# Performance work log

Hardware: AMD Instinct MI355X
Metric: run time of the kernel (lower is better)

The kernel has to match this reference:

```python
import jax, jax.numpy as jnp
import numpy as np

NUM_GROUPS = 32
EPS = 1e-6


def group_norm(x, gamma, beta):
    # x: [B, C, H, W]
    B, C, H, W = x.shape
    xg = x.reshape(B, NUM_GROUPS, C // NUM_GROUPS, H, W)
    mean = jnp.mean(xg, axis=(2, 3, 4), keepdims=True)
    var = jnp.var(xg, axis=(2, 3, 4), keepdims=True)
    xn = ((xg - mean) * jax.lax.rsqrt(var + EPS)).reshape(B, C, H, W)
    return xn * gamma[None, :, None, None] + beta[None, :, None, None]


def conv1x1(x, w, b):
    # x: [B, C, H, W], w: [O, C], b: [O]  (1x1 conv == channel matmul)
    return jnp.einsum('oc,bchw->bohw', w, x) + b[None, :, None, None]


def setup_inputs() -> dict:
    key = jax.random.key(0)
    ks = jax.random.split(key, 10)
    B, C, H, W = 16, 512, 32, 32
    s = 1.0 / np.sqrt(C)
    inp = {
        'hidden_states': jax.random.normal(ks[0], (B, C, H, W), dtype=jnp.float32),
        'norm_gamma': jnp.ones((C,), dtype=jnp.float32),
        'norm_beta': jnp.zeros((C,), dtype=jnp.float32),
        'wq': jax.random.normal(ks[1], (C, C), dtype=jnp.float32) * s,
        'bq': jnp.zeros((C,), dtype=jnp.float32),
        'wk': jax.random.normal(ks[2], (C, C), dtype=jnp.float32) * s,
        'bk': jnp.zeros((C,), dtype=jnp.float32),
        'wv': jax.random.normal(ks[3], (C, C), dtype=jnp.float32) * s,
        'bv': jnp.zeros((C,), dtype=jnp.float32),
        'wo': jax.random.normal(ks[4], (C, C), dtype=jnp.float32) * s,
        'bo': jnp.zeros((C,), dtype=jnp.float32),
    }
    return inp


def reference(hidden_states, norm_gamma, norm_beta, wq, bq, wk, bk, wv, bv, wo, bo):
    residual = hidden_states
    h = group_norm(hidden_states, norm_gamma, norm_beta)
    q = conv1x1(h, wq, bq)  # [B, C, H, W]
    k = conv1x1(h, wk, bk)
    v = conv1x1(h, wv, bv)
    B, C, H, W = q.shape
    N = H * W
    qf = q.reshape(B, C, N)  # [B, C, N]
    kf = k.reshape(B, C, N)
    vf = v.reshape(B, C, N)
    scale = float(C) ** (-0.5)
    # attn_weights[b, i, j] = sum_c q[b,c,i] * k[b,c,j]
    attn = jnp.einsum('bci,bcj->bij', qf, kf) * scale
    attn = jax.nn.softmax(attn, axis=2)
    # out[b, c, i] = sum_j v[b,c,j] * attn[b,i,j]
    out = jnp.einsum('bcj,bij->bci', vf, attn).reshape(B, C, H, W)
    out = conv1x1(out, wo, bo)
    return residual + out
```

## Files before the change

### kernel.cpp

```cpp
#include <hip/hip_runtime.h>

typedef __attribute__((ext_vector_type(4))) float f32x4;
typedef __attribute__((ext_vector_type(8))) __bf16 bf16x8;
typedef __attribute__((ext_vector_type(4))) unsigned short us4;
typedef __attribute__((ext_vector_type(8))) unsigned short us8;

#define B_  16
#define C_  512
#define N_  1024
#define G_  32
#define GS  16

__device__ inline unsigned short f2bf(float f) {
  unsigned u = __builtin_bit_cast(unsigned, f);
  u += 0x7fffu + ((u >> 16) & 1u);
  return (unsigned short)(u >> 16);
}

#define GLOAD_LDS16(gp, lp) __builtin_amdgcn_global_load_lds( \
    (const __attribute__((address_space(1))) unsigned int*)(gp), \
    (__attribute__((address_space(3))) unsigned int*)(lp), 16, 0, 0)

__global__ __launch_bounds__(256) void gn_stats(const float* __restrict__ x,
                                                float* __restrict__ stats) {
  int bg = blockIdx.x;
  const float* xp = x + (long)bg * (GS * N_);
  int tid = threadIdx.x;
  float s = 0.f, ss = 0.f;
  for (int i = tid * 4; i < GS * N_; i += 1024) {
    f32x4 v = *(const f32x4*)&xp[i];
    s += v.x + v.y + v.z + v.w;
    ss += v.x * v.x + v.y * v.y + v.z * v.z + v.w * v.w;
  }
  __shared__ float r1[256], r2[256];
  r1[tid] = s; r2[tid] = ss; __syncthreads();
  for (int off = 128; off > 0; off >>= 1) {
    if (tid < off) { r1[tid] += r1[tid + off]; r2[tid] += r2[tid + off]; }
    __syncthreads();
  }
  if (tid == 0) {
    float mean = r1[0] * (1.f / (GS * N_));
    float var  = r2[0] * (1.f / (GS * N_)) - mean * mean;
    stats[bg * 2]     = mean;
    stats[bg * 2 + 1] = rsqrtf(var + 1e-6f);
  }
}

__global__ __launch_bounds__(256) void gn_apply(const float* __restrict__ x,
                                                const float* __restrict__ stats,
                                                const float* __restrict__ gamma,
                                                const float* __restrict__ beta,
                                                unsigned short* __restrict__ ht) {
  int b = blockIdx.z, ct = blockIdx.y, nt = blockIdx.x;
  int c0 = ct * 64, n0 = nt * 64;
  int tid = threadIdx.x;
  __shared__ unsigned short L[64 * 68];
  const float* xp = x + ((long)b * C_ + c0) * N_ + n0;
#pragma unroll
  for (int i = 0; i < 4; ++i) {
    int li = tid + i * 256;
    int row = li >> 4;
    int col4 = (li & 15) * 4;
    f32x4 v = *(const f32x4*)&xp[(long)row * N_ + col4];
    int c = c0 + row;
    float mean = stats[(b * G_ + (c >> 4)) * 2];
    float rstd = stats[(b * G_ + (c >> 4)) * 2 + 1];
    float gm = gamma[c] * rstd;
    float bt = beta[c] - mean * gm;
    us4 o;
    o.x = f2bf(v.x * gm + bt); o.y = f2bf(v.y * gm + bt);
    o.z = f2bf(v.z * gm + bt); o.w = f2bf(v.w * gm + bt);
    *(us4*)&L[row * 68 + col4] = o;
  }
  __syncthreads();
#pragma unroll
  for (int i = 0; i < 2; ++i) {
    int s = tid + i * 256;
    int n = s >> 3;
    int cs = (s & 7) * 8;
    us8 o;
#pragma unroll
    for (int j = 0; j < 8; ++j) o[j] = L[(cs + j) * 68 + n];
    *(us8*)&ht[((long)b * N_ + n0 + n) * C_ + c0 + cs] = o;
  }
}

__global__ __launch_bounds__(256) void convert_w(const float* __restrict__ wq, const float* __restrict__ wk,
                                                 const float* __restrict__ wo,
                                                 const float* __restrict__ bq, const float* __restrict__ bk,
                                                 const float* __restrict__ bv,
                                                 unsigned short* __restrict__ wqk,
                                                 unsigned short* __restrict__ wob, float* __restrict__ bqk,
                                                 float* __restrict__ bvo) {
  long bid = blockIdx.x;
  int tid = threadIdx.x;
  long i = bid * 256 + tid;
  if (i < C_ * C_) {
    wqk[i]           = f2bf(wq[i]);
    wqk[C_ * C_ + i] = f2bf(wk[i]);
    wob[i]           = f2bf(wo[i]);
  }
  if (i < C_) { bqk[i] = bq[i]; bqk[C_ + i] = bk[i]; }
  if (bid >= 1024) {
    int o = (int)(bid - 1024) * 256 + tid;
    const float* wr = wo + (long)o * 512;
    float acc = 0.f;
    for (int c = 0; c < 512; c += 4) {
      f32x4 w4 = *(const f32x4*)&wr[c];
      f32x4 b4 = *(const f32x4*)&bv[c];
      acc += w4.x * b4.x + w4.y * b4.y + w4.z * b4.z + w4.w * b4.w;
    }
    bvo[o] = acc;
  }
}

__global__ __launch_bounds__(256) void transpose_wv(const float* __restrict__ wv,
                                                    unsigned short* __restrict__ wvT) {
  int c0 = blockIdx.x * 64, k0 = blockIdx.y * 64;
  int tid = threadIdx.x;
  __shared__ float Lt[64][65];
#pragma unroll
  for (int i = 0; i < 4; ++i) {
    int lin = tid + i * 256;
    int rr = lin >> 4;
    int q4 = (lin & 15) * 4;
    f32x4 v = *(const f32x4*)&wv[(long)(c0 + rr) * 512 + k0 + q4];
    Lt[q4 + 0][rr] = v.x; Lt[q4 + 1][rr] = v.y;
    Lt[q4 + 2][rr] = v.z; Lt[q4 + 3][rr] = v.w;
  }
  __syncthreads();
#pragma unroll
  for (int i = 0; i < 2; ++i) {
    int lin = tid + i * 256;
    int kk = lin >> 3;
    int cc = (lin & 7) * 8;
    us8 o;
#pragma unroll
    for (int j = 0; j < 8; ++j) o[j] = f2bf(Lt[kk][cc + j]);
    *(us8*)&wvT[(long)(k0 + kk) * 512 + c0 + cc] = o;
  }
}

__device__ inline f32x4 mfma16(bf16x8 a, bf16x8 b, f32x4 c) {
  return __builtin_amdgcn_mfma_f32_16x16x32_bf16(a, b, c, 0, 0, 0);
}

__global__ __launch_bounds__(256) void wprod(const unsigned short* __restrict__ wob,
                                             const unsigned short* __restrict__ wvT,
                                             unsigned short* __restrict__ WVO) {
  int row0 = blockIdx.x * 64, col0 = blockIdx.y * 64;
  int tid = threadIdx.x, lane = tid & 63, w = tid >> 6;
  int lr = lane & 15, kh = (lane >> 4) * 8;
  f32x4 acc4[4];
#pragma unroll
  for (int n = 0; n < 4; ++n) acc4[n] = f32x4{0.f, 0.f, 0.f, 0.f};
  for (int k0 = 0; k0 < 512; k0 += 32) {
    bf16x8 af = *(const bf16x8*)&wob[(long)(row0 + w * 16 + lr) * 512 + k0 + kh];
#pragma unroll
    for (int n = 0; n < 4; ++n) {
      bf16x8 bf8 = *(const bf16x8*)&wvT[(long)(col0 + n * 16 + lr) * 512 + k0 + kh];
      acc4[n] = mfma16(af, bf8, acc4[n]);
    }
  }
  int rb = (lane >> 4) * 4;
#pragma unroll
  for (int n = 0; n < 4; ++n)
#pragma unroll
    for (int r = 0; r < 4; ++r)
      WVO[(long)(row0 + w * 16 + rb + r) * 512 + col0 + n * 16 + lr] = f2bf(acc4[n][r]);
}

__device__ inline int swz(int b) { return b ^ (((b >> 9) & 1) << 5); }

template<int NREP, int EPI, int XSWZ>
__global__ __launch_bounds__(512, 2) void gemm256(
    const unsigned short* __restrict__ A, long lda, long Az,
    const unsigned short* __restrict__ Bm, long ldb, long Bz,
    void* __restrict__ Dp, long ldd, long Dz,
    const float* __restrict__ bias, float scale, int K,
    const float* __restrict__ residual, float* __restrict__ rs) {
  constexpr int BN = NREP * 64;
  int bx = blockIdx.x, by = blockIdx.y, bz = blockIdx.z;
  if constexpr (XSWZ) {
    int lin = bx + 4 * (by + 4 * bz);
    int l2  = (lin & 7) * 32 + (lin >> 3);
    bx = l2 & 3; by = (l2 >> 2) & 3; bz = l2 >> 4;
  }
  const int z = bz;
  const long row0 = (long)bx * 256;
  const long col0 = (long)by * BN;
  const int tid  = threadIdx.x;
  const int lane = tid & 63;
  const int wave = tid >> 6;
  const int wm = wave >> 2;
  const int wn = wave & 3;
  const int lr = lane & 15;
  const int khb = (lane >> 4) * 16;

  __shared__ unsigned short Abuf[2][16384];
  __shared__ unsigned short Bbuf[2][NREP * 4096];
  __shared__ float sred[256];

  const unsigned short* Ab = A  + (long)z * Az;
  const unsigned short* Bb = Bm + (long)z * Bz;

  if constexpr (EPI == 7) {
    if (tid < 256) {
      const float* rp = rs + ((long)z * 1024 + row0 + tid) * 16;
      float s = 0.f;
#pragma unroll
      for (int i = 0; i < 16; ++i) s += rp[i];
      sred[tid] = 1.f / s;
    }
    asm volatile("s_waitcnt lgkmcnt(0)" ::: "memory");
  }

  const unsigned short* gA[4];
#pragma unroll
  for (int r = 0; r < 4; ++r) {
    int L = swz(r * 8192 + tid * 16);
    gA[r] = Ab + (row0 + (L >> 7)) * lda + ((L & 127) >> 1);
  }
  const unsigned short* gB[NREP];
#pragma unroll
  for (int r = 0; r < NREP; ++r) {
    int L = swz(r * 8192 + tid * 16);
    gB[r] = Bb + (col0 + (L >> 7)) * ldb + ((L & 127) >> 1);
  }

  f32x4 acc[8][NREP];
#pragma unroll
  for (int m = 0; m < 8; ++m)
#pragma unroll
    for (int n = 0; n < NREP; ++n) acc[m][n] = f32x4{0.f, 0.f, 0.f, 0.f};

  const int NT = K >> 6;
#pragma unroll
  for (int r = 0; r < 4; ++r)    GLOAD_LDS16(gA[r], &Abuf[0][r * 4096 + wave * 512]);
#pragma unroll
  for (int r = 0; r < NREP; ++r) GLOAD_LDS16(gB[r], &Bbuf[0][r * 4096 + wave * 512]);

  for (int t = 0; t < NT; ++t) {
    int tn = t + 1; if (tn == NT) tn = 0;
    const long ko = (long)tn << 6;
    const int nb = (t + 1) & 1;
#pragma unroll
    for (int r = 0; r < 4; ++r)    GLOAD_LDS16(gA[r] + ko, &Abuf[nb][r * 4096 + wave * 512]);
#pragma unroll
    for (int r = 0; r < NREP; ++r) GLOAD_LDS16(gB[r] + ko, &Bbuf[nb][r * 4096 + wave * 512]);
    if constexpr (NREP == 4) asm volatile("s_waitcnt vmcnt(8)" ::: "memory");
    else                     asm volatile("s_waitcnt vmcnt(6)" ::: "memory");
    __builtin_amdgcn_s_barrier();
    __builtin_amdgcn_sched_barrier(0);
    const unsigned short* Al = Abuf[t & 1];
    const unsigned short* Bl = Bbuf[t & 1];
#pragma unroll
    for (int kk = 0; kk < 2; ++kk) {
      bf16x8 af[8], bfr[NREP];
#pragma unroll
      for (int m = 0; m < 8; ++m) {
        int Pb = swz((wm * 128 + m * 16 + lr) * 128 + kk * 64 + khb);
        af[m] = *(const bf16x8*)((const char*)Al + Pb);
      }
#pragma unroll
      for (int n = 0; n < NREP; ++n) {
        int Pb = swz((wn * (NREP * 16) + n * 16 + lr) * 128 + kk * 64 + khb);
        bfr[n] = *(const bf16x8*)((const char*)Bl + Pb);
      }
      __builtin_amdgcn_s_setprio(1);
#pragma unroll
      for (int m = 0; m < 8; ++m)
#pragma unroll
        for (int n = 0; n < NREP; ++n)
          acc[m][n] = mfma16(af[m], bfr[n], acc[m][n]);
      __builtin_amdgcn_s_setprio(0);
    }
    __builtin_amdgcn_sched_barrier(0);
    __builtin_amdgcn_s_barrier();
    __builtin_amdgcn_sched_barrier(0);
  }
  asm volatile("s_waitcnt vmcnt(0)" ::: "memory");
  __builtin_amdgcn_s_barrier();

  const int rb = (lane >> 4) * 4;

  if constexpr (EPI == 7) {
#pragma unroll
    for (int m = 0; m < 8; ++m) {
      int lrow = wm * 128 + m * 16 + rb;
      long gr0 = row0 + lrow;
#pragma unroll
      for (int n = 0; n < NREP; ++n) {
        long gc = col0 + wn * (NREP * 16) + n * 16 + lr;
        long o = (long)z * (512L * 1024L) + gc * 1024L + gr0;
        f32x4 res = *(const f32x4*)&residual[o];
        float bb = bias[gc];
        f32x4 st;
#pragma unroll
        for (int r = 0; r < 4; ++r)
          st[r] = acc[m][n][r] * sred[lrow + r] + bb + res[r];
        *(f32x4*)&((float*)Dp)[o] = st;
      }
    }
    return;
  }

  float* slab = ((float*)(void*)Abuf) + wave * 1088;
  const int jt = by;
  unsigned short* Dst = (unsigned short*)Dp + (long)z * Dz;
#pragma unroll
  for (int m = 0; m < 8; ++m) {
    float ps[4] = {0.f, 0.f, 0.f, 0.f};
#pragma unroll
    for (int n = 0; n < NREP; ++n) {
      float bcol = 0.f;
      if constexpr (EPI == 0) bcol = bias[col0 + wn * (NREP * 16) + n * 16 + lr];
#pragma unroll
      for (int r = 0; r < 4; ++r) {
        float v = acc[m][n][r];
        if constexpr (EPI == 0) v += bcol;
        else if constexpr (EPI == 1) v += bias[row0 + wm * 128 + m * 16 + rb + r];
        else if constexpr (EPI == 5) { v = exp2f(v * scale); ps[r] += v; }
        slab[(rb + r) * 68 + n * 16 + lr] = v;
      }
    }
    if constexpr (EPI == 5) {
#pragma unroll
      for (int r = 0; r < 4; ++r) {
        ps[r] += __shfl_xor(ps[r], 1);
        ps[r] += __shfl_xor(ps[r], 2);
        ps[r] += __shfl_xor(ps[r], 4);
        ps[r] += __shfl_xor(ps[r], 8);
      }
      if (lr == 0) {
#pragma unroll
        for (int r = 0; r < 4; ++r)
          rs[((long)z * 1024 + row0 + wm * 128 + m * 16 + rb + r) * 16 + jt * 4 + wn] = ps[r];
      }
    }
    if constexpr (NREP == 4) {
#pragma unroll
      for (int p = 0; p < 2; ++p) {
        int rl = p * 8 + (lane >> 3);
        int c8 = (lane & 7) * 8;
        f32x4 v0 = *(const f32x4*)&slab[rl * 68 + c8];
        f32x4 v1 = *(const f32x4*)&slab[rl * 68 + c8 + 4];
        us8 o;
        o[0] = f2bf(v0.x); o[1] = f2bf(v0.y); o[2] = f2bf(v0.z); o[3] = f2bf(v0.w);
        o[4] = f2bf(v1.x); o[5] = f2bf(v1.y); o[6] = f2bf(v1.z); o[7] = f2bf(v1.w);
        *(us8*)&Dst[(row0 + wm * 128 + m * 16 + rl) * ldd + col0 + wn * 64 + c8] = o;
      }
    } else {
      int rl = lane >> 2;
      int c8 = (lane & 3) * 8;
      f32x4 v0 = *(const f32x4*)&slab[rl * 68 + c8];
      f32x4 v1 = *(const f32x4*)&slab[rl * 68 + c8 + 4];
      us8 o;
      o[0] = f2bf(v0.x); o[1] = f2bf(v0.y); o[2] = f2bf(v0.z); o[3] = f2bf(v0.w);
      o[4] = f2bf(v1.x); o[5] = f2bf(v1.y); o[6] = f2bf(v1.z); o[7] = f2bf(v1.w);
      *(us8*)&Dst[(row0 + wm * 128 + m * 16 + rl) * ldd + col0 + wn * 32 + c8] = o;
    }
  }
}

extern "C" void kernel_launch(void* const* d_in, const int* in_sizes, int n_in,
                              void* d_out, int out_size, void* d_ws, size_t ws_size,
                              hipStream_t stream) {
  const float* x     = (const float*)d_in[0];
  const float* gamma = (const float*)d_in[1];
  const float* beta  = (const float*)d_in[2];
  const float* wq    = (const float*)d_in[3];
  const float* bq    = (const float*)d_in[4];
  const float* wk    = (const float*)d_in[5];
  const float* bk    = (const float*)d_in[6];
  const float* wv    = (const float*)d_in[7];
  const float* bv    = (const float*)d_in[8];
  const float* wo    = (const float*)d_in[9];
  const float* bo    = (const float*)d_in[10];
  float* out = (float*)d_out;

  char* ws = (char*)d_ws;
  unsigned short* ht   = (unsigned short*)(ws + 0);
  unsigned short* qkt  = (unsigned short*)(ws + 16777216);
  unsigned short* VWT  = (unsigned short*)(ws + 50331648);
  unsigned short* S    = (unsigned short*)(ws + 83886080);
  unsigned short* wqkb = (unsigned short*)(ws + 117440512);
  unsigned short* wvT  = (unsigned short*)(ws + 119537664);
  unsigned short* wob  = (unsigned short*)(ws + 120061952);
  unsigned short* WVO  = (unsigned short*)(ws + 120586240);
  float* bqk           = (float*)(ws + 121110528);
  float* bvo           = (float*)(ws + 121114624);
  float* stats         = (float*)(ws + 121116672);
  float* rs            = (float*)(ws + 121122816);

  convert_w<<<1026, 256, 0, stream>>>(wq, wk, wo, bq, bk, bv,
                                      wqkb, wob, bqk, bvo);
  transpose_wv<<<dim3(8, 8), 256, 0, stream>>>(wv, wvT);
  wprod<<<dim3(8, 8), 256, 0, stream>>>(wob, wvT, WVO);
  gn_stats<<<512, 256, 0, stream>>>(x, stats);
  gn_apply<<<dim3(16, 8, 16), 256, 0, stream>>>(x, stats, gamma, beta, ht);

  gemm256<4, 0, 0><<<dim3(64, 4, 1), 512, 0, stream>>>(ht, 512, 0, wqkb, 512, 0,
                                                       qkt, 1024, 0, bqk, 0.f, 512, nullptr, nullptr);
  gemm256<2, 1, 0><<<dim3(2, 128, 1), 512, 0, stream>>>(WVO, 512, 0, ht, 512, 0,
                                                        VWT, 16384, 0, bvo, 0.f, 512, nullptr, nullptr);
  gemm256<4, 5, 1><<<dim3(4, 4, 16), 512, 0, stream>>>(qkt, 1024, 1048576L, qkt + 512, 1024, 1048576L,
                                                       S, 1024, 1048576L, nullptr,
                                                       0.06375871416f, 512, nullptr, rs);
  gemm256<2, 7, 1><<<dim3(4, 4, 16), 512, 0, stream>>>(S, 1024, 1048576L,
                                                       VWT, 16384, 1024,
                                                       out, 0, 0, bo, 0.f, 1024, x, rs);
}
```

Before: 154.6 us.

## Fold Q and K projections into a single precomputed Wq^T·Wk matrix

Instead of projecting h to both Q and K and then computing QK^T, the code precomputes WM = Wq^T·Wk and projects h once to T = h·WM. The score GEMM then computes T·h^T, with per-row and per-column bias terms (alpha, beta) added in its epilogue. This halves the output width of the projection GEMM and shrinks its intermediate buffer. In exchange it adds small kernels for the weight product, the bias vectors and the per-token bias dot products, and it rounds the combined weight matrix to bf16, which may change accuracy.

```diff
diff --git a/kernel.cpp b/kernel.cpp
--- a/kernel.cpp
+++ b/kernel.cpp
@@ -15,6 +15,10 @@
   unsigned u = __builtin_bit_cast(unsigned, f);
   u += 0x7fffu + ((u >> 16) & 1u);
   return (unsigned short)(u >> 16);
+}
+__device__ inline float bf2f(unsigned short u) {
+  unsigned x = (unsigned)u << 16;
+  return __builtin_bit_cast(float, x);
 }
 
 #define GLOAD_LDS16(gp, lp) __builtin_amdgcn_global_load_lds( \
@@ -85,22 +89,14 @@
   }
 }
 
-__global__ __launch_bounds__(256) void convert_w(const float* __restrict__ wq, const float* __restrict__ wk,
-                                                 const float* __restrict__ wo,
-                                                 const float* __restrict__ bq, const float* __restrict__ bk,
+__global__ __launch_bounds__(256) void convert_w(const float* __restrict__ wo,
                                                  const float* __restrict__ bv,
-                                                 unsigned short* __restrict__ wqk,
-                                                 unsigned short* __restrict__ wob, float* __restrict__ bqk,
+                                                 unsigned short* __restrict__ wob,
                                                  float* __restrict__ bvo) {
   long bid = blockIdx.x;
   int tid = threadIdx.x;
   long i = bid * 256 + tid;
-  if (i < C_ * C_) {
-    wqk[i]           = f2bf(wq[i]);
-    wqk[C_ * C_ + i] = f2bf(wk[i]);
-    wob[i]           = f2bf(wo[i]);
-  }
-  if (i < C_) { bqk[i] = bq[i]; bqk[C_ + i] = bk[i]; }
+  if (i < C_ * C_) wob[i] = f2bf(wo[i]);
   if (bid >= 1024) {
     int o = (int)(bid - 1024) * 256 + tid;
     const float* wr = wo + (long)o * 512;
@@ -114,8 +110,14 @@
   }
 }
 
-__global__ __launch_bounds__(256) void transpose_wv(const float* __restrict__ wv,
-                                                    unsigned short* __restrict__ wvT) {
+__global__ __launch_bounds__(256) void transpose3(const float* __restrict__ wq,
+                                                  const float* __restrict__ wk,
+                                                  const float* __restrict__ wv,
+                                                  unsigned short* __restrict__ wqT,
+                                                  unsigned short* __restrict__ wkT,
+                                                  unsigned short* __restrict__ wvT) {
+  const float* src = (blockIdx.z == 0) ? wq : (blockIdx.z == 1) ? wk : wv;
+  unsigned short* dst = (blockIdx.z == 0) ? wqT : (blockIdx.z == 1) ? wkT : wvT;
   int c0 = blockIdx.x * 64, k0 = blockIdx.y * 64;
   int tid = threadIdx.x;
   __shared__ float Lt[64][65];
@@ -124,7 +126,7 @@
     int lin = tid + i * 256;
     int rr = lin >> 4;
     int q4 = (lin & 15) * 4;
-    f32x4 v = *(const f32x4*)&wv[(long)(c0 + rr) * 512 + k0 + q4];
+    f32x4 v = *(const f32x4*)&src[(long)(c0 + rr) * 512 + k0 + q4];
     Lt[q4 + 0][rr] = v.x; Lt[q4 + 1][rr] = v.y;
     Lt[q4 + 2][rr] = v.z; Lt[q4 + 3][rr] = v.w;
   }
@@ -137,7 +139,7 @@
     us8 o;
 #pragma unroll
     for (int j = 0; j < 8; ++j) o[j] = f2bf(Lt[kk][cc + j]);
-    *(us8*)&wvT[(long)(k0 + kk) * 512 + c0 + cc] = o;
+    *(us8*)&dst[(long)(k0 + kk) * 512 + c0 + cc] = o;
   }
 }
 
@@ -145,9 +147,15 @@
   return __builtin_amdgcn_mfma_f32_16x16x32_bf16(a, b, c, 0, 0, 0);
 }
 
-__global__ __launch_bounds__(256) void wprod(const unsigned short* __restrict__ wob,
+__global__ __launch_bounds__(256) void wprod(const unsigned short* __restrict__ wkT,
+                                             const unsigned short* __restrict__ wqT,
+                                             const unsigned short* __restrict__ wob,
                                              const unsigned short* __restrict__ wvT,
+                                             unsigned short* __restrict__ WM,
                                              unsigned short* __restrict__ WVO) {
+  const unsigned short* A = blockIdx.z ? wob : wkT;
+  const unsigned short* B = blockIdx.z ? wvT : wqT;
+  unsigned short* D = blockIdx.z ? WVO : WM;
   int row0 = blockIdx.x * 64, col0 = blockIdx.y * 64;
   int tid = threadIdx.x, lane = tid & 63, w = tid >> 6;
   int lr = lane & 15, kh = (lane >> 4) * 8;
@@ -155,10 +163,10 @@
 #pragma unroll
   for (int n = 0; n < 4; ++n) acc4[n] = f32x4{0.f, 0.f, 0.f, 0.f};
   for (int k0 = 0; k0 < 512; k0 += 32) {
-    bf16x8 af = *(const bf16x8*)&wob[(long)(row0 + w * 16 + lr) * 512 + k0 + kh];
+    bf16x8 af = *(const bf16x8*)&A[(long)(row0 + w * 16 + lr) * 512 + k0 + kh];
 #pragma unroll
     for (int n = 0; n < 4; ++n) {
-      bf16x8 bf8 = *(const bf16x8*)&wvT[(long)(col0 + n * 16 + lr) * 512 + k0 + kh];
+      bf16x8 bf8 = *(const bf16x8*)&B[(long)(col0 + n * 16 + lr) * 512 + k0 + kh];
       acc4[n] = mfma16(af, bf8, acc4[n]);
     }
   }
@@ -167,7 +175,73 @@
   for (int n = 0; n < 4; ++n)
 #pragma unroll
     for (int r = 0; r < 4; ++r)
-      WVO[(long)(row0 + w * 16 + rb + r) * 512 + col0 + n * 16 + lr] = f2bf(acc4[n][r]);
+      D[(long)(row0 + w * 16 + rb + r) * 512 + col0 + n * 16 + lr] = f2bf(acc4[n][r]);
+}
+
+__global__ __launch_bounds__(256) void uv_kernel(const unsigned short* __restrict__ wqT,
+                                                 const unsigned short* __restrict__ wkT,
+                                                 const float* __restrict__ bq,
+                                                 const float* __restrict__ bk,
+                                                 float* __restrict__ u, float* __restrict__ v,
+                                                 float* __restrict__ s0g) {
+  int tid = threadIdx.x, lane = tid & 63, wv_ = tid >> 6;
+  int gw = blockIdx.x * 4 + wv_;
+  int half = gw >> 5;
+  const unsigned short* W = half ? wkT : wqT;
+  const float* bvec = half ? bq : bk;
+  f32x4 b4a = *(const f32x4*)&bvec[lane * 8];
+  f32x4 b4b = *(const f32x4*)&bvec[lane * 8 + 4];
+  for (int rr = 0; rr < 16; ++rr) {
+    int row = (gw & 31) * 16 + rr;
+    us8 w8 = *(const us8*)&W[(long)row * 512 + lane * 8];
+    float d = bf2f(w8[0]) * b4a.x + bf2f(w8[1]) * b4a.y + bf2f(w8[2]) * b4a.z + bf2f(w8[3]) * b4a.w
+            + bf2f(w8[4]) * b4b.x + bf2f(w8[5]) * b4b.y + bf2f(w8[6]) * b4b.z + bf2f(w8[7]) * b4b.w;
+#pragma unroll
+    for (int off = 1; off < 64; off <<= 1) d += __shfl_xor(d, off);
+    if (lane == 0) { if (half) v[row] = d; else u[row] = d; }
+  }
+  if (gw == 0) {
+    f32x4 qa = *(const f32x4*)&bq[lane * 8];
+    f32x4 qb = *(const f32x4*)&bq[lane * 8 + 4];
+    f32x4 ka = *(const f32x4*)&bk[lane * 8];
+    f32x4 kb = *(const f32x4*)&bk[lane * 8 + 4];
+    float d = qa.x * ka.x + qa.y * ka.y + qa.z * ka.z + qa.w * ka.w
+            + qb.x * kb.x + qb.y * kb.y + qb.z * kb.z + qb.w * kb.w;
+#pragma unroll
+    for (int off = 1; off < 64; off <<= 1) d += __shfl_xor(d, off);
+    if (lane == 0) s0g[0] = d;
+  }
+}
+
+__global__ __launch_bounds__(256) void alphabeta(const unsigned short* __restrict__ ht,
+                                                 const float* __restrict__ u,
+                                                 const float* __restrict__ v,
+                                                 const float* __restrict__ s0g,
+                                                 float* __restrict__ alpha,
+                                                 float* __restrict__ betav) {
+  int tid = threadIdx.x, lane = tid & 63, w = tid >> 6;
+  long gw = (long)blockIdx.x * 4 + w;
+  f32x4 ua = *(const f32x4*)&u[lane * 8];
+  f32x4 ub = *(const f32x4*)&u[lane * 8 + 4];
+  f32x4 va = *(const f32x4*)&v[lane * 8];
+  f32x4 vb = *(const f32x4*)&v[lane * 8 + 4];
+  float s0 = s0g[0];
+  for (int rr = 0; rr < 16; ++rr) {
+    long row = gw * 16 + rr;
+    us8 h8 = *(const us8*)&ht[row * 512 + lane * 8];
+    float h0 = bf2f(h8[0]), h1 = bf2f(h8[1]), h2 = bf2f(h8[2]), h3 = bf2f(h8[3]);
+    float h4 = bf2f(h8[4]), h5 = bf2f(h8[5]), h6 = bf2f(h8[6]), h7 = bf2f(h8[7]);
+    float du = h0 * ua.x + h1 * ua.y + h2 * ua.z + h3 * ua.w
+             + h4 * ub.x + h5 * ub.y + h6 * ub.z + h7 * ub.w;
+    float dv = h0 * va.x + h1 * va.y + h2 * va.z + h3 * va.w
+             + h4 * vb.x + h5 * vb.y + h6 * vb.z + h7 * vb.w;
+#pragma unroll
+    for (int off = 1; off < 64; off <<= 1) {
+      du += __shfl_xor(du, off);
+      dv += __shfl_xor(dv, off);
+    }
+    if (lane == 0) { alpha[row] = s0 + du; betav[row] = dv; }
+  }
 }
 
 __device__ inline int swz(int b) { return b ^ (((b >> 9) & 1) << 5); }
@@ -308,19 +382,28 @@
   float* slab = ((float*)(void*)Abuf) + wave * 1088;
   const int jt = by;
   unsigned short* Dst = (unsigned short*)Dp + (long)z * Dz;
+  float bc[NREP];
+  if constexpr (EPI == 5) {
+#pragma unroll
+    for (int n = 0; n < NREP; ++n)
+      bc[n] = residual[(long)z * 1024 + col0 + wn * (NREP * 16) + n * 16 + lr];
+  }
 #pragma unroll
   for (int m = 0; m < 8; ++m) {
     float ps[4] = {0.f, 0.f, 0.f, 0.f};
+    float ar[4];
+    if constexpr (EPI == 5) {
+#pragma unroll
+      for (int r = 0; r < 4; ++r)
+        ar[r] = bias[(long)z * 1024 + row0 + wm * 128 + m * 16 + rb + r];
+    }
 #pragma unroll
     for (int n = 0; n < NREP; ++n) {
-      float bcol = 0.f;
-      if constexpr (EPI == 0) bcol = bias[col0 + wn * (NREP * 16) + n * 16 + lr];
 #pragma unroll
       for (int r = 0; r < 4; ++r) {
         float v = acc[m][n][r];
-        if constexpr (EPI == 0) v += bcol;
-        else if constexpr (EPI == 1) v += bias[row0 + wm * 128 + m * 16 + rb + r];
-        else if constexpr (EPI == 5) { v = exp2f(v * scale); ps[r] += v; }
+        if constexpr (EPI == 1) v += bias[row0 + wm * 128 + m * 16 + rb + r];
+        else if constexpr (EPI == 5) { v = exp2f((v + ar[r] + bc[n]) * scale); ps[r] += v; }
         slab[(rb + r) * 68 + n * 16 + lr] = v;
       }
     }
@@ -381,32 +464,39 @@
 
   char* ws = (char*)d_ws;
   unsigned short* ht   = (unsigned short*)(ws + 0);
-  unsigned short* qkt  = (unsigned short*)(ws + 16777216);
-  unsigned short* VWT  = (unsigned short*)(ws + 50331648);
-  unsigned short* S    = (unsigned short*)(ws + 83886080);
-  unsigned short* wqkb = (unsigned short*)(ws + 117440512);
-  unsigned short* wvT  = (unsigned short*)(ws + 119537664);
-  unsigned short* wob  = (unsigned short*)(ws + 120061952);
-  unsigned short* WVO  = (unsigned short*)(ws + 120586240);
-  float* bqk           = (float*)(ws + 121110528);
-  float* bvo           = (float*)(ws + 121114624);
-  float* stats         = (float*)(ws + 121116672);
-  float* rs            = (float*)(ws + 121122816);
-
-  convert_w<<<1026, 256, 0, stream>>>(wq, wk, wo, bq, bk, bv,
-                                      wqkb, wob, bqk, bvo);
-  transpose_wv<<<dim3(8, 8), 256, 0, stream>>>(wv, wvT);
-  wprod<<<dim3(8, 8), 256, 0, stream>>>(wob, wvT, WVO);
+  unsigned short* T    = (unsigned short*)(ws + 16777216);
+  unsigned short* VWT  = (unsigned short*)(ws + 33554432);
+  unsigned short* S    = (unsigned short*)(ws + 50331648);
+  unsigned short* wqT  = (unsigned short*)(ws + 83886080);
+  unsigned short* wkT  = (unsigned short*)(ws + 84410368);
+  unsigned short* wvT  = (unsigned short*)(ws + 84934656);
+  unsigned short* wob  = (unsigned short*)(ws + 85458944);
+  unsigned short* WM   = (unsigned short*)(ws + 85983232);
+  unsigned short* WVO  = (unsigned short*)(ws + 86507520);
+  float* u             = (float*)(ws + 87031808);
+  float* v             = (float*)(ws + 87033856);
+  float* s0g           = (float*)(ws + 87035904);
+  float* bvo           = (float*)(ws + 87037952);
+  float* stats         = (float*)(ws + 87040000);
+  float* alpha         = (float*)(ws + 87046144);
+  float* betav         = (float*)(ws + 87111680);
+  float* rs            = (float*)(ws + 87177216);
+
+  convert_w<<<1026, 256, 0, stream>>>(wo, bv, wob, bvo);
+  transpose3<<<dim3(8, 8, 3), 256, 0, stream>>>(wq, wk, wv, wqT, wkT, wvT);
+  wprod<<<dim3(8, 8, 2), 256, 0, stream>>>(wkT, wqT, wob, wvT, WM, WVO);
+  uv_kernel<<<16, 256, 0, stream>>>(wqT, wkT, bq, bk, u, v, s0g);
   gn_stats<<<512, 256, 0, stream>>>(x, stats);
   gn_apply<<<dim3(16, 8, 16), 256, 0, stream>>>(x, stats, gamma, beta, ht);
-
-  gemm256<4, 0, 0><<<dim3(64, 4, 1), 512, 0, stream>>>(ht, 512, 0, wqkb, 512, 0,
-                                                       qkt, 1024, 0, bqk, 0.f, 512, nullptr, nullptr);
+  alphabeta<<<256, 256, 0, stream>>>(ht, u, v, s0g, alpha, betav);
+
+  gemm256<2, 3, 0><<<dim3(64, 4, 1), 512, 0, stream>>>(ht, 512, 0, WM, 512, 0,
+                                                       T, 512, 0, nullptr, 0.f, 512, nullptr, nullptr);
   gemm256<2, 1, 0><<<dim3(2, 128, 1), 512, 0, stream>>>(WVO, 512, 0, ht, 512, 0,
                                                         VWT, 16384, 0, bvo, 0.f, 512, nullptr, nullptr);
-  gemm256<4, 5, 1><<<dim3(4, 4, 16), 512, 0, stream>>>(qkt, 1024, 1048576L, qkt + 512, 1024, 1048576L,
-                                                       S, 1024, 1048576L, nullptr,
-                                                       0.06375871416f, 512, nullptr, rs);
+  gemm256<4, 5, 1><<<dim3(4, 4, 16), 512, 0, stream>>>(T, 512, 524288L, ht, 512, 524288L,
+                                                       S, 1024, 1048576L, alpha,
+                                                       0.06375871416f, 512, betav, rs);
   gemm256<2, 7, 1><<<dim3(4, 4, 16), 512, 0, stream>>>(S, 1024, 1048576L,
                                                        VWT, 16384, 1024,
                                                        out, 0, 0, bo, 0.f, 1024, x, rs);
```

Result: slower. 166.3 us (+7.5%).
